# Optimization experiments

Hardware: AMD Instinct MI355X
Metric: run time of the kernel (lower is better)

The kernel has to match this reference:

```python
import jax, jax.numpy as jnp
import numpy as np

N_TOTAL_USERS = 200000
N_TOTAL_ITEMS = 300000
N_DOM_USERS = 60000
N_DOM_ITEMS = 90000
N_DOMAINS = 3
DIM = 32           # hidden_dim // 2
N_LAYERS = 2
ALPHA = 0.1


def grec_conv(src, dst, x, n_nodes):
    """LightGCN-style propagation with APPNP residual (alpha), symmetric norm.
    Edge dropout is disabled (eval mode). x: [n_nodes, d]."""
    ones = jnp.ones(src.shape[0], dtype=x.dtype)
    deg = jax.ops.segment_sum(ones, dst, num_segments=n_nodes)
    inv_sqrt = jax.lax.rsqrt(jnp.maximum(deg, 1.0))
    w = inv_sqrt[src] * inv_sqrt[dst]            # [E] edge norm
    h = x
    for _ in range(N_LAYERS):
        msg = h[src] * w[:, None]                # gather + scale, [E, d]
        agg = jax.ops.segment_sum(msg, dst, num_segments=n_nodes)
        h = (1.0 - ALPHA) * agg + ALPHA * x      # residual to layer-0 emb
    return h


def setup_inputs() -> dict:
    key = jax.random.key(0)
    ks = jax.random.split(key, 8)
    return {
        "dom_edges": jax.random.randint(ks[0], (2, 2000000), 0, N_DOM_USERS + N_DOM_ITEMS, dtype=jnp.int32),
        "sep_edges": jax.random.randint(ks[1], (3, 2, 2000000), 0, N_TOTAL_USERS + N_TOTAL_ITEMS, dtype=jnp.int32),
        "aggr_user_w": 0.1 * jax.random.normal(ks[2], (N_TOTAL_USERS, DIM), dtype=jnp.float32),
        "aggr_item_w": 0.1 * jax.random.normal(ks[3], (N_TOTAL_ITEMS, DIM), dtype=jnp.float32),
        "dom_user_w": 0.1 * jax.random.normal(ks[4], (N_DOM_USERS, DIM), dtype=jnp.float32),
        "dom_item_w": 0.1 * jax.random.normal(ks[5], (N_DOM_ITEMS, DIM), dtype=jnp.float32),
        "user_ids_dom": jnp.arange(N_DOM_USERS, dtype=jnp.int32),
        "item_ids_dom": jnp.arange(N_DOM_ITEMS, dtype=jnp.int32),
        "users": jax.random.randint(ks[6], (8192,), 0, N_DOM_USERS).astype(jnp.int64),
        "items": jax.random.randint(ks[7], (8192,), 0, N_DOM_ITEMS).astype(jnp.int64),
    }


def reference(dom_edges, sep_edges, aggr_user_w, aggr_item_w,
              dom_user_w, dom_item_w, user_ids_dom, item_ids_dom,
              users, items):
    n_dom_nodes = N_DOM_USERS + N_DOM_ITEMS
    n_all_nodes = N_TOTAL_USERS + N_TOTAL_ITEMS

    # ---- intra-domain conv (mode='dis_intra') on the domain graph ----
    x_intra = jnp.concatenate([dom_user_w, dom_item_w], axis=0)
    h_intra = grec_conv(dom_edges[0], dom_edges[1], x_intra, n_dom_nodes)
    user_intra = h_intra[:N_DOM_USERS]
    item_intra = h_intra[N_DOM_USERS:]

    # ---- inter-domain conv (mode='dis_inter'): per-domain sep graphs, mean ----
    x_inter = jnp.concatenate([aggr_user_w, aggr_item_w], axis=0)
    embs = []
    for d in range(N_DOMAINS):  # small fixed loop over domains
        h = grec_conv(sep_edges[d, 0], sep_edges[d, 1], x_inter, n_all_nodes)
        uss = h[:N_TOTAL_USERS][user_ids_dom]   # gather this domain's users
        its = h[N_TOTAL_USERS:][item_ids_dom]   # gather this domain's items
        embs.append(jnp.concatenate([uss, its], axis=0))
    light_out = jnp.mean(jnp.stack(embs, axis=1), axis=1)  # [n_dom_nodes, DIM]
    user_inter = light_out[:N_DOM_USERS]
    item_inter = light_out[N_DOM_USERS:]

    # ---- concat inter || intra, score query pairs ----
    all_users = jnp.concatenate([user_inter, user_intra], axis=1)  # [Nu_d, 64]
    all_items = jnp.concatenate([item_inter, item_intra], axis=1)
    users_emb = all_users[users]
    items_emb = all_items[items]
    gamma = jnp.sum(users_emb * items_emb, axis=1)  # [B]
    return gamma
```

## Files before the change

kernel.cpp:

```cpp
#include <hip/hip_runtime.h>


static constexpr int NTU = 200000, NTI = 300000, NDU = 60000, NDI = 90000;
static constexpr int NDOMN = 150000, NALLN = 500000, NE = 2000000;
static constexpr int DIM = 32, NQ = 8192;
static constexpr int TN = NDOMN + 3 * NALLN;

static constexpr int BSH_I = 9,  BN_I = 512,  NBK_I = 293, CAP_I = 7680;
static constexpr int BSH_E = 11, BN_E = 2048, NBK_E = 245, CAP_E = 9216;
static constexpr int GEW_I = NBK_I * CAP_I;
static constexpr int GEW_E = NBK_E * CAP_E;
static constexpr int GEW   = GEW_I + 3 * GEW_E;
static constexpr int NBCK  = NBK_I + 3 * NBK_E;
static constexpr int ACT_CAP = 360000;
static constexpr int PCHUNK = 4096;
static constexpr int PBLK_PG = (NE + PCHUNK - 1) / PCHUNK;

static constexpr size_t a256(size_t x) { return (x + 255) & ~(size_t)255; }
static constexpr size_t O_NEED  = 0;
static constexpr size_t O_N1    = a256((size_t)NDOMN * 4);
static constexpr size_t ZB      = O_N1 + a256(TN);
static constexpr size_t O_RANK  = ZB;
static constexpr size_t O_BSUM  = O_RANK + a256((size_t)NDOMN * 4);
static constexpr size_t O_BCUR  = O_BSUM + 1024;
static constexpr size_t O_DEG8  = O_BCUR + a256(NBCK * 4);
static constexpr size_t O_OFF   = O_DEG8 + a256(TN);
static constexpr size_t O_RANK1 = O_OFF  + a256((size_t)TN * 4);
static constexpr size_t O_ALIST = O_RANK1 + a256((size_t)TN * 4);
static constexpr size_t O_NLIST = O_ALIST + a256((size_t)ACT_CAP * 4);
static constexpr size_t O_GE    = O_NLIST + a256((size_t)16384 * 4);
static constexpr size_t O_AGG1  = O_GE   + (size_t)GEW * 4;
static constexpr size_t O_A2    = O_AGG1 + (size_t)ACT_CAP * DIM * 4;

__global__ void k_setup(uint4* __restrict__ zp, int n16, unsigned* __restrict__ bcur) {
    int t = blockIdx.x * blockDim.x + threadIdx.x;
    if (t < n16) zp[t] = make_uint4(0u, 0u, 0u, 0u);
    if (t < NBCK) {
        int g, b;
        if (t < NBK_I) { g = 0; b = t; }
        else { int r = t - NBK_I; g = 1 + r / NBK_E; b = r - (g - 1) * NBK_E; }
        unsigned geb = (g == 0) ? 0u : (unsigned)(GEW_I + (g - 1) * GEW_E);
        unsigned cap = (g == 0) ? CAP_I : CAP_E;
        bcur[t] = geb + (unsigned)b * cap;
    }
}

__global__ void k_scatter_needed(const int* __restrict__ users, const int* __restrict__ items,
                                 unsigned* __restrict__ need) {
    int t = blockIdx.x * blockDim.x + threadIdx.x;
    if (t < NQ)            need[users[t]] = 1u;
    else if (t < 2 * NQ)   need[NDU + items[t - NQ]] = 1u;
}

__global__ __launch_bounds__(256, 6) void k_part(const int* __restrict__ dom, const int* __restrict__ sep,
                                                 unsigned* __restrict__ bcur,
                                                 unsigned* __restrict__ gE) {
    __shared__ unsigned hist[512], lstart[512], gbase[512];
    __shared__ unsigned wsum[4];
    int t = threadIdx.x;
    int g = blockIdx.x / PBLK_PG;
    int chunk = blockIdx.x - g * PBLK_PG;
    const int* src = (g == 0) ? dom : sep + (size_t)(g - 1) * 2 * NE;
    const int* dst = src + NE;
    int bsh = (g == 0) ? BSH_I : BSH_E;
    unsigned bnm = (g == 0) ? (BN_I - 1) : (BN_E - 1);
    int nbk = (g == 0) ? NBK_I : NBK_E;
    unsigned cap = (g == 0) ? CAP_I : CAP_E;
    unsigned geb = (g == 0) ? 0u : (unsigned)(GEW_I + (g - 1) * GEW_E);
    int bco = (g == 0) ? 0 : NBK_I + (g - 1) * NBK_E;
    hist[t] = 0u; hist[t + 256] = 0u;
    __syncthreads();
    int vbase = chunk * (PCHUNK / 4);
    unsigned pk[16]; unsigned short bb[16];
    #pragma unroll
    for (int i = 0; i < 4; i++) {
        int vi = vbase + i * 256 + t;
        if (vi < NE / 4) {
            int4 sv = ((const int4*)src)[vi];
            int4 dv = ((const int4*)dst)[vi];
            int ss[4] = {sv.x, sv.y, sv.z, sv.w};
            int dd[4] = {dv.x, dv.y, dv.z, dv.w};
            #pragma unroll
            for (int e = 0; e < 4; e++) {
                unsigned d = (unsigned)dd[e];
                unsigned b = d >> bsh;
                pk[i * 4 + e] = ((d & bnm) << 19) | (unsigned)ss[e];
                bb[i * 4 + e] = (unsigned short)b;
                atomicAdd(&hist[b], 1u);
            }
        } else {
            #pragma unroll
            for (int e = 0; e < 4; e++) bb[i * 4 + e] = 0xFFFF;
        }
    }
    __syncthreads();
    unsigned c0 = hist[2 * t], c1 = hist[2 * t + 1], ps = c0 + c1;
    int lane = t & 63, wid = t >> 6;
    unsigned x = ps;
    #pragma unroll
    for (int o = 1; o < 64; o <<= 1) {
        unsigned y = __shfl_up(x, o);
        if (lane >= o) x += y;
    }
    if (lane == 63) wsum[wid] = x;
    __syncthreads();
    unsigned wo = 0;
    if (wid > 0) wo += wsum[0];
    if (wid > 1) wo += wsum[1];
    if (wid > 2) wo += wsum[2];
    x += wo;
    unsigned e0 = x - ps, e1 = e0 + c0;
    lstart[2 * t] = e0; lstart[2 * t + 1] = e1;
    hist[2 * t] = e0; hist[2 * t + 1] = e1;
    if (2 * t < nbk && c0) {
        unsigned gb = atomicAdd(&bcur[bco + 2 * t], c0);
        gbase[2 * t] = (gb + c0 <= geb + (unsigned)(2 * t + 1) * cap) ? gb : 0xFFFFFFFFu;
    }
    if (2 * t + 1 < nbk && c1) {
        unsigned gb = atomicAdd(&bcur[bco + 2 * t + 1], c1);
        gbase[2 * t + 1] = (gb + c1 <= geb + (unsigned)(2 * t + 2) * cap) ? gb : 0xFFFFFFFFu;
    }
    __syncthreads();
    #pragma unroll
    for (int i = 0; i < 16; i++) {
        if (bb[i] != 0xFFFF) {
            unsigned b = bb[i];
            unsigned p = atomicAdd(&hist[b], 1u);
            unsigned gb = gbase[b];
            if (gb != 0xFFFFFFFFu) gE[gb + (p - lstart[b])] = pk[i];
        }
    }
}

__global__ __launch_bounds__(256) void k_sortb(unsigned* __restrict__ gE,
                                               const unsigned* __restrict__ bcur,
                                               unsigned* __restrict__ off,
                                               unsigned char* __restrict__ deg8) {
    __shared__ unsigned ed[CAP_E];
    __shared__ unsigned h2[BN_E];
    __shared__ unsigned scanarr[256];
    int t = threadIdx.x, bx = blockIdx.x;
    int g, b;
    if (bx < NBK_I) { g = 0; b = bx; }
    else { int r = bx - NBK_I; g = 1 + r / NBK_E; b = r - (g - 1) * NBK_E; }
    int bn = (g == 0) ? BN_I : BN_E;
    unsigned cap = (g == 0) ? CAP_I : CAP_E;
    unsigned geb = (g == 0) ? 0u : (unsigned)(GEW_I + (g - 1) * GEW_E);
    int bco = (g == 0) ? 0 : NBK_I + (g - 1) * NBK_E;
    int nb = (g == 0) ? 0 : NDOMN + (g - 1) * NALLN;
    int nnodes = (g == 0) ? NDOMN : NALLN;
    unsigned j0 = geb + (unsigned)b * cap;
    unsigned cnt = bcur[bco + b] - j0;
    if (cnt > cap) cnt = cap;
    for (unsigned j = t; j < cnt; j += 256) ed[j] = gE[j0 + j];
    for (int k = t; k < bn; k += 256) h2[k] = 0u;
    __syncthreads();
    for (unsigned j = t; j < cnt; j += 256) atomicAdd(&h2[ed[j] >> 19], 1u);
    __syncthreads();
    int E = bn >> 8;
    unsigned c[8], pre[8]; unsigned ssum = 0;
    int k0 = t * E;
    for (int q = 0; q < E; q++) { c[q] = h2[k0 + q]; pre[q] = ssum; ssum += c[q]; }
    scanarr[t] = ssum;
    unsigned x = ssum;
    for (int o = 1; o < 256; o <<= 1) {
        __syncthreads();
        unsigned y = (t >= o) ? scanarr[t - o] : 0u;
        __syncthreads();
        x += y; scanarr[t] = x;
    }
    __syncthreads();
    unsigned excl = x - ssum;
    int vb = b * bn;
    for (int q = 0; q < E; q++) {
        int v = vb + k0 + q;
        if (v < nnodes) { off[nb + v] = j0 + excl + pre[q]; deg8[nb + v] = (unsigned char)c[q]; }
    }
    for (int q = 0; q < E; q++) h2[k0 + q] = excl + pre[q];
    __syncthreads();
    for (unsigned j = t; j < cnt; j += 256) {
        unsigned e = ed[j];
        unsigned p = atomicAdd(&h2[e >> 19], 1u);
        gE[j0 + p] = e & 0x7FFFFu;
    }
}

__global__ void k_mark(const unsigned* __restrict__ need, const unsigned* __restrict__ off,
                       const unsigned char* __restrict__ deg8, const unsigned* __restrict__ gE,
                       unsigned char* __restrict__ n1) {
    int t = blockIdx.x * blockDim.x + threadIdx.x;
    if (t >= 4 * NDOMN) return;
    int v = t >> 2, g = t & 3;
    if (!need[v]) return;
    int nb, node;
    if (g == 0) { nb = 0; node = v; }
    else { nb = NDOMN + (g - 1) * NALLN; node = (v < NDU) ? v : NTU + (v - NDU); }
    int gv = nb + node;
    unsigned j0 = off[gv];
    int dg = deg8[gv];
    unsigned char* n1g = n1 + nb;
    for (int j = 0; j < dg; j++) n1g[gE[j0 + j]] = 1;
}

static constexpr int SCAN_T = 256;

template <int EL, typename T>
__global__ void k_scan1(const T* __restrict__ in, unsigned* __restrict__ out,
                        unsigned* __restrict__ bsum, int n) {
    __shared__ unsigned lds[SCAN_T];
    int b = blockIdx.x, t = threadIdx.x;
    int base = b * (SCAN_T * EL) + t * EL;
    unsigned v[EL]; unsigned s = 0;
    for (int i = 0; i < EL; i++) { int idx = base + i; v[i] = (idx < n) ? (unsigned)in[idx] : 0u; s += v[i]; }
    lds[t] = s;
    unsigned x = s;
    for (int o = 1; o < SCAN_T; o <<= 1) {
        __syncthreads();
        unsigned y = (t >= o) ? lds[t - o] : 0u;
        __syncthreads();
        x += y; lds[t] = x;
    }
    unsigned running = x - s;
    for (int i = 0; i < EL; i++) { int idx = base + i; if (idx < n) out[idx] = running; running += v[i]; }
    if (t == SCAN_T - 1) bsum[b] = x;
}

__global__ void k_scan2(unsigned* __restrict__ bsum, int nbv) {
    __shared__ unsigned lds[SCAN_T];
    int t = threadIdx.x;
    unsigned s = (t < nbv) ? bsum[t] : 0u;
    lds[t] = s;
    unsigned x = s;
    for (int o = 1; o < SCAN_T; o <<= 1) {
        __syncthreads();
        unsigned y = (t >= o) ? lds[t - o] : 0u;
        __syncthreads();
        x += y; lds[t] = x;
    }
    if (t < nbv) bsum[t] = x - s;
}

template <int CH>
__global__ void k_scan3(unsigned* __restrict__ out, const unsigned* __restrict__ bsum, int n) {
    int i = blockIdx.x * blockDim.x + threadIdx.x;
    if (i < n) out[i] += bsum[i / CH];
}

__global__ void k_lists(const unsigned char* __restrict__ n1, const unsigned* __restrict__ rank1,
                        unsigned* __restrict__ alist,
                        const unsigned* __restrict__ need, const unsigned* __restrict__ rank,
                        unsigned* __restrict__ nlist) {
    int t = blockIdx.x * blockDim.x + threadIdx.x;
    if (t < TN && n1[t]) { unsigned r = rank1[t]; if (r < ACT_CAP) alist[r] = (unsigned)t; }
    if (t < NDOMN && need[t]) nlist[rank[t]] = (unsigned)t;
}

__global__ void k_gather1(const unsigned* __restrict__ alist, const unsigned* __restrict__ off,
                          const unsigned char* __restrict__ deg8, const unsigned* __restrict__ gE,
                          const float* __restrict__ auw, const float* __restrict__ aiw,
                          const float* __restrict__ duw, const float* __restrict__ diw,
                          float* __restrict__ agg1) {
    int t = blockIdx.x * blockDim.x + threadIdx.x;
    int r = t >> 3, c = t & 7;
    if (r >= ACT_CAP) return;
    unsigned gv = alist[r];
    if (gv >= (unsigned)TN) return;
    int g, nb;
    if ((int)gv < NDOMN) { g = 0; nb = 0; }
    else { int q = (int)gv - NDOMN; g = 1 + q / NALLN; nb = NDOMN + (g - 1) * NALLN; }
    int v = (int)gv - nb;
    const float* uw = g ? auw : duw;
    const float* iw = g ? aiw : diw;
    int UB = g ? NTU : NDU;
    const unsigned char* d8 = deg8 + nb;
    unsigned j0 = off[gv];
    int dg = deg8[gv];
    float invd = rsqrtf(fmaxf((float)dg, 1.0f));
    float4 acc = make_float4(0.f, 0.f, 0.f, 0.f);
    int j = 0;
    for (; j + 4 <= dg; j += 4) {
        int s0 = (int)gE[j0 + j], s1 = (int)gE[j0 + j + 1];
        int s2 = (int)gE[j0 + j + 2], s3 = (int)gE[j0 + j + 3];
        float4 x0 = ((const float4*)((s0 < UB) ? uw + (size_t)s0 * DIM : iw + (size_t)(s0 - UB) * DIM))[c];
        float4 x1 = ((const float4*)((s1 < UB) ? uw + (size_t)s1 * DIM : iw + (size_t)(s1 - UB) * DIM))[c];
        float4 x2 = ((const float4*)((s2 < UB) ? uw + (size_t)s2 * DIM : iw + (size_t)(s2 - UB) * DIM))[c];
        float4 x3 = ((const float4*)((s3 < UB) ? uw + (size_t)s3 * DIM : iw + (size_t)(s3 - UB) * DIM))[c];
        float w0 = rsqrtf(fmaxf((float)d8[s0], 1.0f)) * invd;
        float w1 = rsqrtf(fmaxf((float)d8[s1], 1.0f)) * invd;
        float w2 = rsqrtf(fmaxf((float)d8[s2], 1.0f)) * invd;
        float w3 = rsqrtf(fmaxf((float)d8[s3], 1.0f)) * invd;
        acc.x += w0 * x0.x + w1 * x1.x + w2 * x2.x + w3 * x3.x;
        acc.y += w0 * x0.y + w1 * x1.y + w2 * x2.y + w3 * x3.y;
        acc.z += w0 * x0.z + w1 * x1.z + w2 * x2.z + w3 * x3.z;
        acc.w += w0 * x0.w + w1 * x1.w + w2 * x2.w + w3 * x3.w;
    }
    for (; j < dg; j++) {
        int s = (int)gE[j0 + j];
        float w = rsqrtf(fmaxf((float)d8[s], 1.0f)) * invd;
        float4 xv = ((const float4*)((s < UB) ? uw + (size_t)s * DIM : iw + (size_t)(s - UB) * DIM))[c];
        acc.x += w * xv.x; acc.y += w * xv.y; acc.z += w * xv.z; acc.w += w * xv.w;
    }
    float4 xo = ((const float4*)((v < UB) ? uw + (size_t)v * DIM : iw + (size_t)(v - UB) * DIM))[c];
    float4 A;
    A.x = 0.9f * acc.x + 0.1f * xo.x;
    A.y = 0.9f * acc.y + 0.1f * xo.y;
    A.z = 0.9f * acc.z + 0.1f * xo.z;
    A.w = 0.9f * acc.w + 0.1f * xo.w;
    ((float4*)(agg1 + (size_t)r * DIM))[c] = A;
}

__global__ void k_gather2(const unsigned* __restrict__ nlist, const unsigned* __restrict__ rank,
                          const unsigned* __restrict__ rank1, const unsigned* __restrict__ off,
                          const unsigned char* __restrict__ deg8, const unsigned* __restrict__ gE,
                          const float* __restrict__ agg1, float* __restrict__ a2) {
    int t = blockIdx.x * blockDim.x + threadIdx.x;
    int idx = t >> 3, c = t & 7;
    int g = idx >> 14;
    int r = idx & 16383;
    unsigned v = nlist[r];
    if (v >= (unsigned)NDOMN) return;
    int nb, node;
    if (g == 0) { nb = 0; node = (int)v; }
    else { nb = NDOMN + (g - 1) * NALLN; node = ((int)v < NDU) ? (int)v : NTU + ((int)v - NDU); }
    int gv = nb + node;
    unsigned j0 = off[gv];
    int dg = deg8[gv];
    float invd = rsqrtf(fmaxf((float)dg, 1.0f));
    const unsigned char* d8 = deg8 + nb;
    const unsigned* r1 = rank1 + nb;
    float4 acc = make_float4(0.f, 0.f, 0.f, 0.f);
    int j = 0;
    for (; j + 4 <= dg; j += 4) {
        int s0 = (int)gE[j0 + j], s1 = (int)gE[j0 + j + 1];
        int s2 = (int)gE[j0 + j + 2], s3 = (int)gE[j0 + j + 3];
        unsigned a0 = r1[s0], a1 = r1[s1], a2i = r1[s2], a3 = r1[s3];
        float4 A0 = ((const float4*)(agg1 + (size_t)a0 * DIM))[c];
        float4 A1 = ((const float4*)(agg1 + (size_t)a1 * DIM))[c];
        float4 A2 = ((const float4*)(agg1 + (size_t)a2i * DIM))[c];
        float4 A3 = ((const float4*)(agg1 + (size_t)a3 * DIM))[c];
        float w0 = rsqrtf(fmaxf((float)d8[s0], 1.0f)) * invd;
        float w1 = rsqrtf(fmaxf((float)d8[s1], 1.0f)) * invd;
        float w2 = rsqrtf(fmaxf((float)d8[s2], 1.0f)) * invd;
        float w3 = rsqrtf(fmaxf((float)d8[s3], 1.0f)) * invd;
        acc.x += w0 * A0.x + w1 * A1.x + w2 * A2.x + w3 * A3.x;
        acc.y += w0 * A0.y + w1 * A1.y + w2 * A2.y + w3 * A3.y;
        acc.z += w0 * A0.z + w1 * A1.z + w2 * A2.z + w3 * A3.z;
        acc.w += w0 * A0.w + w1 * A1.w + w2 * A2.w + w3 * A3.w;
    }
    for (; j < dg; j++) {
        int s = (int)gE[j0 + j];
        unsigned ar = r1[s];
        float w = rsqrtf(fmaxf((float)d8[s], 1.0f)) * invd;
        float4 A = ((const float4*)(agg1 + (size_t)ar * DIM))[c];
        acc.x += w * A.x; acc.y += w * A.y; acc.z += w * A.z; acc.w += w * A.w;
    }
    ((float4*)(a2 + ((size_t)g * 16384 + rank[v]) * DIM))[c] = acc;
}

__global__ void k_gamma(const int* __restrict__ users, const int* __restrict__ items,
                        const unsigned* __restrict__ rank, const float* __restrict__ a2,
                        const float* __restrict__ auw, const float* __restrict__ aiw,
                        const float* __restrict__ duw, const float* __restrict__ diw,
                        float* __restrict__ out) {
    int t = blockIdx.x * blockDim.x + threadIdx.x;
    int q = t >> 3;
    if (q >= NQ) return;
    int c = t & 7;
    int u = users[q], it = items[q];
    int ru = (int)rank[u], ri = (int)rank[NDU + it];
    auto A2 = [&](int g, int r) { return ((const float4*)(a2 + ((size_t)g * 16384 + r) * DIM))[c]; };
    float4 Du = A2(0, ru), Di = A2(0, ri);
    float4 U1 = A2(1, ru), U2 = A2(2, ru), U3 = A2(3, ru);
    float4 V1 = A2(1, ri), V2 = A2(2, ri), V3 = A2(3, ri);
    float4 xu = ((const float4*)(auw + (size_t)u * DIM))[c];
    float4 xi = ((const float4*)(aiw + (size_t)it * DIM))[c];
    float4 yu = ((const float4*)(duw + (size_t)u * DIM))[c];
    float4 yi = ((const float4*)(diw + (size_t)it * DIM))[c];
    float s = 0.f;
    s += (0.3f * (U1.x + U2.x + U3.x) + 0.1f * xu.x) * (0.3f * (V1.x + V2.x + V3.x) + 0.1f * xi.x);
    s += (0.3f * (U1.y + U2.y + U3.y) + 0.1f * xu.y) * (0.3f * (V1.y + V2.y + V3.y) + 0.1f * xi.y);
    s += (0.3f * (U1.z + U2.z + U3.z) + 0.1f * xu.z) * (0.3f * (V1.z + V2.z + V3.z) + 0.1f * xi.z);
    s += (0.3f * (U1.w + U2.w + U3.w) + 0.1f * xu.w) * (0.3f * (V1.w + V2.w + V3.w) + 0.1f * xi.w);
    s += (0.9f * Du.x + 0.1f * yu.x) * (0.9f * Di.x + 0.1f * yi.x);
    s += (0.9f * Du.y + 0.1f * yu.y) * (0.9f * Di.y + 0.1f * yi.y);
    s += (0.9f * Du.z + 0.1f * yu.z) * (0.9f * Di.z + 0.1f * yi.z);
    s += (0.9f * Du.w + 0.1f * yu.w) * (0.9f * Di.w + 0.1f * yi.w);
    s += __shfl_xor(s, 1);
    s += __shfl_xor(s, 2);
    s += __shfl_xor(s, 4);
    if (c == 0) out[q] = s;
}

extern "C" void kernel_launch(void* const* d_in, const int* in_sizes, int n_in,
                              void* d_out, int out_size, void* d_ws, size_t ws_size,
                              hipStream_t stream) {
    const int*   dom_edges = (const int*)d_in[0];
    const int*   sep_edges = (const int*)d_in[1];
    const float* auw       = (const float*)d_in[2];
    const float* aiw       = (const float*)d_in[3];
    const float* duw       = (const float*)d_in[4];
    const float* diw       = (const float*)d_in[5];
    const int*   users     = (const int*)d_in[8];
    const int*   items     = (const int*)d_in[9];
    float*       out       = (float*)d_out;

    char* ws = (char*)d_ws;
    unsigned*      need  = (unsigned*)(ws + O_NEED);
    unsigned char* n1    = (unsigned char*)(ws + O_N1);
    unsigned*      rank  = (unsigned*)(ws + O_RANK);
    unsigned*      bsum  = (unsigned*)(ws + O_BSUM);
    unsigned*      bcur  = (unsigned*)(ws + O_BCUR);
    unsigned char* deg8  = (unsigned char*)(ws + O_DEG8);
    unsigned*      off   = (unsigned*)(ws + O_OFF);
    unsigned*      rank1 = (unsigned*)(ws + O_RANK1);
    unsigned*      alist = (unsigned*)(ws + O_ALIST);
    unsigned*      nlist = (unsigned*)(ws + O_NLIST);
    unsigned*      gE    = (unsigned*)(ws + O_GE);
    float*         agg1  = (float*)(ws + O_AGG1);
    float*         a2    = (float*)(ws + O_A2);

    const int BLK = 256;
    auto cdiv = [](long a, long b) { return (int)((a + b - 1) / b); };

    int n16 = (int)(ZB / 16);
    k_setup<<<cdiv(n16, BLK), BLK, 0, stream>>>((uint4*)ws, n16, bcur);
    k_scatter_needed<<<cdiv(2 * NQ, BLK), BLK, 0, stream>>>(users, items, need);

    {
        int nbv = cdiv(NDOMN, SCAN_T * 8);
        k_scan1<8, unsigned><<<nbv, SCAN_T, 0, stream>>>(need, rank, bsum, NDOMN);
        k_scan2<<<1, SCAN_T, 0, stream>>>(bsum, nbv);
        k_scan3<SCAN_T * 8><<<cdiv(NDOMN, BLK), BLK, 0, stream>>>(rank, bsum, NDOMN);
    }

    k_part<<<4 * PBLK_PG, 256, 0, stream>>>(dom_edges, sep_edges, bcur, gE);

    k_sortb<<<NBCK, 256, 0, stream>>>(gE, bcur, off, deg8);

    k_mark<<<cdiv((long)4 * NDOMN, BLK), BLK, 0, stream>>>(need, off, deg8, gE, n1);

    {
        int nbv = cdiv(TN, SCAN_T * 32);
        k_scan1<32, unsigned char><<<nbv, SCAN_T, 0, stream>>>(n1, rank1, bsum, TN);
        k_scan2<<<1, SCAN_T, 0, stream>>>(bsum, nbv);
        k_scan3<SCAN_T * 32><<<cdiv(TN, BLK), BLK, 0, stream>>>(rank1, bsum, TN);
    }

    k_lists<<<cdiv(TN, BLK), BLK, 0, stream>>>(n1, rank1, alist, need, rank, nlist);

    k_gather1<<<cdiv((long)ACT_CAP * 8, BLK), BLK, 0, stream>>>(alist, off, deg8, gE,
                                                                auw, aiw, duw, diw, agg1);
    k_gather2<<<cdiv((long)4 * 16384 * 8, BLK), BLK, 0, stream>>>(nlist, rank, rank1, off, deg8,
                                                                  gE, agg1, a2);

    k_gamma<<<cdiv((long)NQ * 8, BLK), BLK, 0, stream>>>(users, items, rank, a2,
                                                         auw, aiw, duw, diw, out);
}
```

Baseline: 403.5 us.

## Simplify edge partition, use warp-shuffle scans, compact marking via need-list

The partition kernel now uses 512-thread blocks over 8192-edge chunks. Each edge's slot is taken with a single LDS atomic in the first pass and packed with its bucket id, which removes the intra-block scan and the second round of atomics. LDS Hillis-Steele scans in the sort and scan kernels are replaced by a wavefront-shuffle block scan. Marking now iterates over the compact needed-node list instead of all domain nodes, and the active-list build is fused into the final scan-add kernel. The costs are larger blocks, a slot field limited to 13 bits, and a non-deterministic edge order within each bucket.

```diff
diff --git a/kernel.cpp b/kernel.cpp
--- a/kernel.cpp
+++ b/kernel.cpp
@@ -13,7 +13,8 @@
 static constexpr int GEW   = GEW_I + 3 * GEW_E;
 static constexpr int NBCK  = NBK_I + 3 * NBK_E;
 static constexpr int ACT_CAP = 360000;
-static constexpr int PCHUNK = 4096;
+static constexpr int BLKP = 512;
+static constexpr int PCHUNK = 8192;
 static constexpr int PBLK_PG = (NE + PCHUNK - 1) / PCHUNK;
 
 static constexpr size_t a256(size_t x) { return (x + 255) & ~(size_t)255; }
@@ -32,6 +33,23 @@
 static constexpr size_t O_AGG1  = O_GE   + (size_t)GEW * 4;
 static constexpr size_t O_A2    = O_AGG1 + (size_t)ACT_CAP * DIM * 4;
 
+__device__ __forceinline__ unsigned blockScanIncl256(unsigned s, unsigned* wsum4, int t) {
+    int lane = t & 63, wid = t >> 6;
+    unsigned x = s;
+    #pragma unroll
+    for (int o = 1; o < 64; o <<= 1) {
+        unsigned y = __shfl_up(x, o);
+        if (lane >= o) x += y;
+    }
+    if (lane == 63) wsum4[wid] = x;
+    __syncthreads();
+    unsigned wo = 0;
+    if (wid > 0) wo += wsum4[0];
+    if (wid > 1) wo += wsum4[1];
+    if (wid > 2) wo += wsum4[2];
+    return x + wo;
+}
+
 __global__ void k_setup(uint4* __restrict__ zp, int n16, unsigned* __restrict__ bcur) {
     int t = blockIdx.x * blockDim.x + threadIdx.x;
     if (t < n16) zp[t] = make_uint4(0u, 0u, 0u, 0u);
@@ -52,11 +70,17 @@
     else if (t < 2 * NQ)   need[NDU + items[t - NQ]] = 1u;
 }
 
-__global__ __launch_bounds__(256, 6) void k_part(const int* __restrict__ dom, const int* __restrict__ sep,
-                                                 unsigned* __restrict__ bcur,
-                                                 unsigned* __restrict__ gE) {
-    __shared__ unsigned hist[512], lstart[512], gbase[512];
-    __shared__ unsigned wsum[4];
+__global__ void k_nlist(const unsigned* __restrict__ need, const unsigned* __restrict__ rank,
+                        unsigned* __restrict__ nlist) {
+    int t = blockIdx.x * blockDim.x + threadIdx.x;
+    if (t < NDOMN && need[t]) nlist[rank[t]] = (unsigned)t;
+}
+
+__global__ __launch_bounds__(BLKP, 8) void k_part(const int* __restrict__ dom,
+                                                  const int* __restrict__ sep,
+                                                  unsigned* __restrict__ bcur,
+                                                  unsigned* __restrict__ gE) {
+    __shared__ unsigned hist[512], gbase[512];
     int t = threadIdx.x;
     int g = blockIdx.x / PBLK_PG;
     int chunk = blockIdx.x - g * PBLK_PG;
@@ -68,13 +92,13 @@
     unsigned cap = (g == 0) ? CAP_I : CAP_E;
     unsigned geb = (g == 0) ? 0u : (unsigned)(GEW_I + (g - 1) * GEW_E);
     int bco = (g == 0) ? 0 : NBK_I + (g - 1) * NBK_E;
-    hist[t] = 0u; hist[t + 256] = 0u;
+    hist[t] = 0u;
     __syncthreads();
     int vbase = chunk * (PCHUNK / 4);
-    unsigned pk[16]; unsigned short bb[16];
+    unsigned pk[16], bp[16];
     #pragma unroll
     for (int i = 0; i < 4; i++) {
-        int vi = vbase + i * 256 + t;
+        int vi = vbase + i * BLKP + t;
         if (vi < NE / 4) {
             int4 sv = ((const int4*)src)[vi];
             int4 dv = ((const int4*)dst)[vi];
@@ -84,50 +108,31 @@
             for (int e = 0; e < 4; e++) {
                 unsigned d = (unsigned)dd[e];
                 unsigned b = d >> bsh;
+                unsigned p = atomicAdd(&hist[b], 1u);
                 pk[i * 4 + e] = ((d & bnm) << 19) | (unsigned)ss[e];
-                bb[i * 4 + e] = (unsigned short)b;
-                atomicAdd(&hist[b], 1u);
+                bp[i * 4 + e] = (b << 13) | p;
             }
         } else {
             #pragma unroll
-            for (int e = 0; e < 4; e++) bb[i * 4 + e] = 0xFFFF;
+            for (int e = 0; e < 4; e++) bp[i * 4 + e] = 0xFFFFFFFFu;
         }
     }
     __syncthreads();
-    unsigned c0 = hist[2 * t], c1 = hist[2 * t + 1], ps = c0 + c1;
-    int lane = t & 63, wid = t >> 6;
-    unsigned x = ps;
-    #pragma unroll
-    for (int o = 1; o < 64; o <<= 1) {
-        unsigned y = __shfl_up(x, o);
-        if (lane >= o) x += y;
-    }
-    if (lane == 63) wsum[wid] = x;
-    __syncthreads();
-    unsigned wo = 0;
-    if (wid > 0) wo += wsum[0];
-    if (wid > 1) wo += wsum[1];
-    if (wid > 2) wo += wsum[2];
-    x += wo;
-    unsigned e0 = x - ps, e1 = e0 + c0;
-    lstart[2 * t] = e0; lstart[2 * t + 1] = e1;
-    hist[2 * t] = e0; hist[2 * t + 1] = e1;
-    if (2 * t < nbk && c0) {
-        unsigned gb = atomicAdd(&bcur[bco + 2 * t], c0);
-        gbase[2 * t] = (gb + c0 <= geb + (unsigned)(2 * t + 1) * cap) ? gb : 0xFFFFFFFFu;
-    }
-    if (2 * t + 1 < nbk && c1) {
-        unsigned gb = atomicAdd(&bcur[bco + 2 * t + 1], c1);
-        gbase[2 * t + 1] = (gb + c1 <= geb + (unsigned)(2 * t + 2) * cap) ? gb : 0xFFFFFFFFu;
+    if (t < nbk) {
+        unsigned c = hist[t];
+        if (c) {
+            unsigned gb = atomicAdd(&bcur[bco + t], c);
+            gbase[t] = (gb + c <= geb + (unsigned)(t + 1) * cap) ? gb : 0xFFFFFFFFu;
+        }
     }
     __syncthreads();
     #pragma unroll
     for (int i = 0; i < 16; i++) {
-        if (bb[i] != 0xFFFF) {
-            unsigned b = bb[i];
-            unsigned p = atomicAdd(&hist[b], 1u);
+        unsigned bpv = bp[i];
+        if (bpv != 0xFFFFFFFFu) {
+            unsigned b = bpv >> 13, p = bpv & 8191u;
             unsigned gb = gbase[b];
-            if (gb != 0xFFFFFFFFu) gE[gb + (p - lstart[b])] = pk[i];
+            if (gb != 0xFFFFFFFFu) gE[gb + p] = pk[i];
         }
     }
 }
@@ -138,7 +143,7 @@
                                                unsigned char* __restrict__ deg8) {
     __shared__ unsigned ed[CAP_E];
     __shared__ unsigned h2[BN_E];
-    __shared__ unsigned scanarr[256];
+    __shared__ unsigned wsum4[4];
     int t = threadIdx.x, bx = blockIdx.x;
     int g, b;
     if (bx < NBK_I) { g = 0; b = bx; }
@@ -161,15 +166,7 @@
     unsigned c[8], pre[8]; unsigned ssum = 0;
     int k0 = t * E;
     for (int q = 0; q < E; q++) { c[q] = h2[k0 + q]; pre[q] = ssum; ssum += c[q]; }
-    scanarr[t] = ssum;
-    unsigned x = ssum;
-    for (int o = 1; o < 256; o <<= 1) {
-        __syncthreads();
-        unsigned y = (t >= o) ? scanarr[t - o] : 0u;
-        __syncthreads();
-        x += y; scanarr[t] = x;
-    }
-    __syncthreads();
+    unsigned x = blockScanIncl256(ssum, wsum4, t);
     unsigned excl = x - ssum;
     int vb = b * bn;
     for (int q = 0; q < E; q++) {
@@ -185,16 +182,17 @@
     }
 }
 
-__global__ void k_mark(const unsigned* __restrict__ need, const unsigned* __restrict__ off,
+__global__ void k_mark(const unsigned* __restrict__ nlist, const unsigned* __restrict__ off,
                        const unsigned char* __restrict__ deg8, const unsigned* __restrict__ gE,
                        unsigned char* __restrict__ n1) {
     int t = blockIdx.x * blockDim.x + threadIdx.x;
-    if (t >= 4 * NDOMN) return;
-    int v = t >> 2, g = t & 3;
-    if (!need[v]) return;
+    if (t >= 4 * 16384) return;
+    int r = t >> 2, g = t & 3;
+    unsigned v = nlist[r];
+    if (v >= (unsigned)NDOMN) return;
     int nb, node;
-    if (g == 0) { nb = 0; node = v; }
-    else { nb = NDOMN + (g - 1) * NALLN; node = (v < NDU) ? v : NTU + (v - NDU); }
+    if (g == 0) { nb = 0; node = (int)v; }
+    else { nb = NDOMN + (g - 1) * NALLN; node = ((int)v < NDU) ? (int)v : NTU + ((int)v - NDU); }
     int gv = nb + node;
     unsigned j0 = off[gv];
     int dg = deg8[gv];
@@ -207,36 +205,22 @@
 template <int EL, typename T>
 __global__ void k_scan1(const T* __restrict__ in, unsigned* __restrict__ out,
                         unsigned* __restrict__ bsum, int n) {
-    __shared__ unsigned lds[SCAN_T];
+    __shared__ unsigned wsum4[4];
     int b = blockIdx.x, t = threadIdx.x;
     int base = b * (SCAN_T * EL) + t * EL;
     unsigned v[EL]; unsigned s = 0;
     for (int i = 0; i < EL; i++) { int idx = base + i; v[i] = (idx < n) ? (unsigned)in[idx] : 0u; s += v[i]; }
-    lds[t] = s;
-    unsigned x = s;
-    for (int o = 1; o < SCAN_T; o <<= 1) {
-        __syncthreads();
-        unsigned y = (t >= o) ? lds[t - o] : 0u;
-        __syncthreads();
-        x += y; lds[t] = x;
-    }
+    unsigned x = blockScanIncl256(s, wsum4, t);
     unsigned running = x - s;
     for (int i = 0; i < EL; i++) { int idx = base + i; if (idx < n) out[idx] = running; running += v[i]; }
     if (t == SCAN_T - 1) bsum[b] = x;
 }
 
 __global__ void k_scan2(unsigned* __restrict__ bsum, int nbv) {
-    __shared__ unsigned lds[SCAN_T];
+    __shared__ unsigned wsum4[4];
     int t = threadIdx.x;
     unsigned s = (t < nbv) ? bsum[t] : 0u;
-    lds[t] = s;
-    unsigned x = s;
-    for (int o = 1; o < SCAN_T; o <<= 1) {
-        __syncthreads();
-        unsigned y = (t >= o) ? lds[t - o] : 0u;
-        __syncthreads();
-        x += y; lds[t] = x;
-    }
+    unsigned x = blockScanIncl256(s, wsum4, t);
     if (t < nbv) bsum[t] = x - s;
 }
 
@@ -246,13 +230,16 @@
     if (i < n) out[i] += bsum[i / CH];
 }
 
-__global__ void k_lists(const unsigned char* __restrict__ n1, const unsigned* __restrict__ rank1,
-                        unsigned* __restrict__ alist,
-                        const unsigned* __restrict__ need, const unsigned* __restrict__ rank,
-                        unsigned* __restrict__ nlist) {
-    int t = blockIdx.x * blockDim.x + threadIdx.x;
-    if (t < TN && n1[t]) { unsigned r = rank1[t]; if (r < ACT_CAP) alist[r] = (unsigned)t; }
-    if (t < NDOMN && need[t]) nlist[rank[t]] = (unsigned)t;
+template <int CH>
+__global__ void k_scan3f(unsigned* __restrict__ rank1, const unsigned* __restrict__ bsum,
+                         const unsigned char* __restrict__ n1, unsigned* __restrict__ alist,
+                         int n) {
+    int i = blockIdx.x * blockDim.x + threadIdx.x;
+    if (i < n) {
+        unsigned r = rank1[i] + bsum[i / CH];
+        rank1[i] = r;
+        if (n1[i] && r < ACT_CAP) alist[r] = (unsigned)i;
+    }
 }
 
 __global__ void k_gather1(const unsigned* __restrict__ alist, const unsigned* __restrict__ off,
@@ -432,21 +419,20 @@
         k_scan2<<<1, SCAN_T, 0, stream>>>(bsum, nbv);
         k_scan3<SCAN_T * 8><<<cdiv(NDOMN, BLK), BLK, 0, stream>>>(rank, bsum, NDOMN);
     }
-
-    k_part<<<4 * PBLK_PG, 256, 0, stream>>>(dom_edges, sep_edges, bcur, gE);
+    k_nlist<<<cdiv(NDOMN, BLK), BLK, 0, stream>>>(need, rank, nlist);
+
+    k_part<<<4 * PBLK_PG, BLKP, 0, stream>>>(dom_edges, sep_edges, bcur, gE);
 
     k_sortb<<<NBCK, 256, 0, stream>>>(gE, bcur, off, deg8);
 
-    k_mark<<<cdiv((long)4 * NDOMN, BLK), BLK, 0, stream>>>(need, off, deg8, gE, n1);
+    k_mark<<<cdiv((long)4 * 16384, BLK), BLK, 0, stream>>>(nlist, off, deg8, gE, n1);
 
     {
         int nbv = cdiv(TN, SCAN_T * 32);
         k_scan1<32, unsigned char><<<nbv, SCAN_T, 0, stream>>>(n1, rank1, bsum, TN);
         k_scan2<<<1, SCAN_T, 0, stream>>>(bsum, nbv);
-        k_scan3<SCAN_T * 32><<<cdiv(TN, BLK), BLK, 0, stream>>>(rank1, bsum, TN);
-    }
-
-    k_lists<<<cdiv(TN, BLK), BLK, 0, stream>>>(n1, rank1, alist, need, rank, nlist);
+        k_scan3f<SCAN_T * 32><<<cdiv(TN, BLK), BLK, 0, stream>>>(rank1, bsum, n1, alist, TN);
+    }
 
     k_gather1<<<cdiv((long)ACT_CAP * 8, BLK), BLK, 0, stream>>>(alist, off, deg8, gE,
                                                                 auw, aiw, duw, diw, agg1);
```

Result: faster. 376.4 us (-6.7%).
